# Optimization experiments

Hardware: AMD Instinct MI355X
Metric: run time of the kernel (lower is better)

## Reference

```python
import jax, jax.numpy as jnp
import numpy as np

N_NODES = 50000
N_EDGES = 800000
F_IN = 64
HID = 64
N_CLASSES = 10
N_GRAPHS = 64


def setup_inputs() -> dict:
    key = jax.random.key(0)
    ks = jax.random.split(key, 16)
    x = jax.random.normal(ks[0], (N_NODES, F_IN), dtype=jnp.float32)
    edge_index = jax.random.randint(ks[1], (2, N_EDGES), 0, N_NODES, dtype=jnp.int32)
    supernode_mask = jax.random.bernoulli(ks[2], 0.1, (N_NODES,))
    edge_mask = jax.random.bernoulli(ks[3], 0.5, (N_EDGES,)).astype(jnp.float32)
    batch = jnp.sort(jax.random.randint(ks[4], (N_NODES,), 0, N_GRAPHS, dtype=jnp.int32))
    def glorot(k, fan_in, fan_out):
        s = jnp.sqrt(6.0 / (fan_in + fan_out))
        return jax.random.uniform(k, (fan_in, fan_out), jnp.float32, -s, s)
    W1 = glorot(ks[5], F_IN, HID); b1 = jnp.zeros((HID,), jnp.float32)
    W2 = glorot(ks[6], HID, HID); b2 = jnp.zeros((HID,), jnp.float32)
    W3 = glorot(ks[7], HID, HID); b3 = jnp.zeros((HID,), jnp.float32)
    Wl = glorot(ks[8], HID, N_CLASSES); bl = jnp.zeros((N_CLASSES,), jnp.float32)
    return {"x": x, "edge_index": edge_index, "supernode_mask": supernode_mask,
            "edge_mask": edge_mask, "batch": batch,
            "W1": W1, "b1": b1, "W2": W2, "b2": b2, "W3": W3, "b3": b3,
            "Wl": Wl, "bl": bl}


def reference(x, edge_index, supernode_mask, edge_mask, batch,
              W1, b1, W2, b2, W3, b3, Wl, bl):
    N = x.shape[0]
    src, dst = edge_index[0], edge_index[1]

    # SimpleConv('add'): weighted sum of source features into targets
    x2 = jax.ops.segment_sum(x[src] * edge_mask[:, None], dst, num_segments=N)
    x = jnp.where(supernode_mask[:, None], x2, x)

    # GCN normalization with self-loops: deg = 1 + in-degree, norm = d^-1/2[src]*d^-1/2[dst]
    deg = jax.ops.segment_sum(jnp.ones((src.shape[0],), x.dtype), dst, num_segments=N) + 1.0
    dinv = jax.lax.rsqrt(deg)
    coef = dinv[src] * dinv[dst]          # [E]
    self_coef = (dinv * dinv)[:, None]    # self-loop contribution [N,1]

    def gcn(h, W, b):
        h = h @ W  # small GEMM [N, HID]
        agg = jax.ops.segment_sum(h[src] * coef[:, None], dst, num_segments=N)
        return agg + h * self_coef + b

    h = jax.nn.relu(gcn(x, W1, b1))
    h = jax.nn.relu(gcn(h, W2, b2))
    h = gcn(h, W3, b3)

    # global_mean_pool over graphs
    sums = jax.ops.segment_sum(h, batch, num_segments=N_GRAPHS)
    cnt = jax.ops.segment_sum(jnp.ones((N,), h.dtype), batch, num_segments=N_GRAPHS)
    pooled = sums / jnp.maximum(cnt, 1.0)[:, None]

    # dropout is identity in eval mode
    return pooled @ Wl + bl
```

## Files before the change

kernel.cpp:

```cpp
#include <hip/hip_runtime.h>

#define FEAT 64
#define NGRAPH 64
#define POOL_CHUNKS 8
#define LAYER_BLOCKS 2048


__device__ __forceinline__ unsigned int pack_bf16(float a, float b) {
    unsigned int ua = __float_as_uint(a), ub = __float_as_uint(b);
    ua = (ua + 0x7FFFu + ((ua >> 16) & 1u)) >> 16;
    ub = (ub + 0x7FFFu + ((ub >> 16) & 1u)) >> 16;
    return ua | (ub << 16);
}
__device__ __forceinline__ float bf_lo(unsigned int w) {
    return __uint_as_float(w << 16);
}
__device__ __forceinline__ float bf_hi(unsigned int w) {
    return __uint_as_float(w & 0xFFFF0000u);
}

__global__ __launch_bounds__(256) void k_init(int* __restrict__ cnt_int,
                                              float* __restrict__ pooled,
                                              int* __restrict__ flag, int N) {
    int i = blockIdx.x * 256 + threadIdx.x;
    if (i < N) cnt_int[i] = 0;
    if (i < NGRAPH * FEAT) pooled[i] = 0.f;
    if (i == 0) *flag = 0;
}

__global__ __launch_bounds__(256) void k_detect(const unsigned int* __restrict__ m,
                                                int nwords, int* __restrict__ flag) {
    int i = blockIdx.x * 256 + threadIdx.x;
    if (i >= nwords) return;
    unsigned int w = m[i];
    if (w == 0x3F800000u) atomicOr(flag, 2);
    else if (w > 1u) atomicOr(flag, 1);
}

__device__ __forceinline__ bool read_mask(const void* sm, int i, int fl) {
    if (fl & 2) return ((const float*)sm)[i] != 0.f;
    if (fl & 1) return ((const unsigned char*)sm)[i] != 0;
    return ((const int*)sm)[i] != 0;
}

__global__ __launch_bounds__(256) void k_count(const int* __restrict__ ei,
                                               int* __restrict__ cnt_int,
                                               int* __restrict__ rank, int E) {
    int e = blockIdx.x * 256 + threadIdx.x;
    if (e >= E) return;
    rank[e] = atomicAdd(&cnt_int[ei[E + e]], 1);
}

__global__ __launch_bounds__(256) void k_scan1(const int* __restrict__ cnt,
                                               int* __restrict__ rowptr,
                                               int* __restrict__ bsum, int N) {
    __shared__ int woff[4];
    int t = threadIdx.x, lane = t & 63, wid = t >> 6;
    int i = blockIdx.x * 256 + t;
    int orig = (i < N) ? cnt[i] : 0;
    int v = orig;
#pragma unroll
    for (int off = 1; off < 64; off <<= 1) {
        int u = __shfl_up(v, off);
        if (lane >= off) v += u;
    }
    if (lane == 63) woff[wid] = v;
    __syncthreads();
    if (t == 0) {
        int a = 0;
#pragma unroll
        for (int w = 0; w < 4; ++w) { int b = woff[w]; woff[w] = a; a += b; }
    }
    __syncthreads();
    int excl = woff[wid] + v - orig;
    if (i < N) rowptr[i] = excl;
    if (t == 255) bsum[blockIdx.x] = woff[3] + v;
}

__global__ __launch_bounds__(256) void k_scan2(int* __restrict__ bsum, int nb) {
    __shared__ int woff[4];
    int t = threadIdx.x, lane = t & 63, wid = t >> 6;
    int orig = (t < nb) ? bsum[t] : 0;
    int v = orig;
#pragma unroll
    for (int off = 1; off < 64; off <<= 1) {
        int u = __shfl_up(v, off);
        if (lane >= off) v += u;
    }
    if (lane == 63) woff[wid] = v;
    __syncthreads();
    if (t == 0) {
        int a = 0;
#pragma unroll
        for (int w = 0; w < 4; ++w) { int b = woff[w]; woff[w] = a; a += b; }
    }
    __syncthreads();
    if (t < nb) bsum[t] = woff[wid] + v - orig;
}

__global__ __launch_bounds__(256) void k_scan3(const int* __restrict__ cnt,
                                               const int* __restrict__ bsum,
                                               int* __restrict__ rowptr,
                                               float* __restrict__ dinv,
                                               int N, int E) {
    int i = blockIdx.x * 256 + threadIdx.x;
    if (i >= N) return;
    rowptr[i] += bsum[blockIdx.x];
    dinv[i] = rsqrtf((float)cnt[i] + 1.0f);
    if (i == 0) rowptr[N] = E;
}

__global__ __launch_bounds__(256) void k_fill(const int* __restrict__ ei,
                                              const float* __restrict__ emask,
                                              const int* __restrict__ rowptr,
                                              const int* __restrict__ rank,
                                              unsigned int* __restrict__ csr, int E) {
    int e = blockIdx.x * 256 + threadIdx.x;
    if (e >= E) return;
    int dst = ei[E + e];
    unsigned int word = (unsigned int)ei[e];
    if (emask[e] != 0.f) word |= 0x10000u;
    csr[rowptr[dst] + rank[e]] = word;
}

__global__ __launch_bounds__(256) void k_sup(const float* __restrict__ x,
                                             const int* __restrict__ rowptr,
                                             const unsigned int* __restrict__ csr,
                                             const void* __restrict__ sm,
                                             const int* __restrict__ flag,
                                             const float* __restrict__ dinv,
                                             unsigned int* __restrict__ u, int N) {
    int t = blockIdx.x * 256 + threadIdx.x;
    int i = t >> 6, lane = t & 63;
    if (i >= N) return;
    int g = lane >> 4, q = lane & 15;
    int fl = *flag;
    float4 acc;
    if (read_mask(sm, i, fl)) {
        int r0 = rowptr[i], r1 = rowptr[i + 1];
        acc.x = 0.f; acc.y = 0.f; acc.z = 0.f; acc.w = 0.f;
        for (int j0 = r0; j0 < r1; j0 += 64) {
            int cnt = min(64, r1 - j0);
            unsigned int w_l = (lane < cnt) ? csr[j0 + lane] : 0u;
            int rounds4 = (cnt + 3) & ~3;
#pragma unroll 2
            for (int j = 0; j < rounds4; j += 4) {
                unsigned int wd = __shfl(w_l, j + g);
                if (wd & 0x10000u) {
                    int s = (int)(wd & 0xFFFFu);
                    const float4 v = *(const float4*)(x + (size_t)s * FEAT + q * 4);
                    acc.x += v.x; acc.y += v.y; acc.z += v.z; acc.w += v.w;
                }
            }
        }
#pragma unroll
        for (int m = 16; m < 64; m <<= 1) {
            acc.x += __shfl_xor(acc.x, m);
            acc.y += __shfl_xor(acc.y, m);
            acc.z += __shfl_xor(acc.z, m);
            acc.w += __shfl_xor(acc.w, m);
        }
    } else {
        acc = *(const float4*)(x + (size_t)i * FEAT + q * 4);
    }
    if (g == 0) {
        float dd = dinv[i];
        uint2 p;
        p.x = pack_bf16(acc.x * dd, acc.y * dd);
        p.y = pack_bf16(acc.z * dd, acc.w * dd);
        *(uint2*)(u + (size_t)i * 32 + q * 2) = p;
    }
}

__global__ __launch_bounds__(256, 4) void k_layer(const unsigned int* __restrict__ u,
                                                  const float* __restrict__ W,
                                                  const float* __restrict__ bias,
                                                  const float* __restrict__ dinv,
                                                  const int* __restrict__ rowptr,
                                                  const unsigned int* __restrict__ csr,
                                                  unsigned int* __restrict__ u_out,
                                                  float* __restrict__ h_out,
                                                  int N, int mode) {
    __shared__ float s_lds[4][64];
    int t = threadIdx.x, lane = t & 63, wid = t >> 6;
    int g = lane >> 4, q = lane & 15;
    float w[64];
#pragma unroll
    for (int k = 0; k < 64; ++k) w[k] = W[k * 64 + lane];
    float bl_ = bias[lane];
    for (int i = blockIdx.x * 4 + wid; i < N; i += LAYER_BLOCKS * 4) {
        int r0 = rowptr[i], r1 = rowptr[i + 1];
        float4 acc = {0.f, 0.f, 0.f, 0.f};
        if (g == 0) {
            const uint2 v = *(const uint2*)(u + (size_t)i * 32 + q * 2);
            acc.x += bf_lo(v.x); acc.y += bf_hi(v.x);
            acc.z += bf_lo(v.y); acc.w += bf_hi(v.y);
        }
        for (int j0 = r0; j0 < r1; j0 += 64) {
            int cnt = min(64, r1 - j0);
            int s_l = (lane < cnt) ? (int)(csr[j0 + lane] & 0xFFFFu) : 0;
            int rounds4 = (cnt + 3) & ~3;
#pragma unroll 4
            for (int j = 0; j < rounds4; j += 4) {
                int jj = j + g;
                int s = __shfl(s_l, jj);
                if (jj < cnt) {
                    const uint2 v = *(const uint2*)(u + (size_t)s * 32 + q * 2);
                    acc.x += bf_lo(v.x); acc.y += bf_hi(v.x);
                    acc.z += bf_lo(v.y); acc.w += bf_hi(v.y);
                }
            }
        }
#pragma unroll
        for (int m = 16; m < 64; m <<= 1) {
            acc.x += __shfl_xor(acc.x, m);
            acc.y += __shfl_xor(acc.y, m);
            acc.z += __shfl_xor(acc.z, m);
            acc.w += __shfl_xor(acc.w, m);
        }
        if (g == 0) *(float4*)(&s_lds[wid][q * 4]) = acc;
        float y = 0.f;
#pragma unroll
        for (int k4 = 0; k4 < 16; ++k4) {
            const float4 sv = *(const float4*)(&s_lds[wid][k4 * 4]);
            y += sv.x * w[k4 * 4 + 0] + sv.y * w[k4 * 4 + 1] +
                 sv.z * w[k4 * 4 + 2] + sv.w * w[k4 * 4 + 3];
        }
        float dd = dinv[i];
        y = y * dd + bl_;
        if (mode == 0) {
            y = fmaxf(y, 0.f);
            float up = y * dd;
            float other = __shfl_xor(up, 1);
            if ((lane & 1) == 0)
                u_out[(size_t)i * 32 + (lane >> 1)] = pack_bf16(up, other);
        } else {
            h_out[(size_t)i * FEAT + lane] = y;
        }
    }
}

__device__ __forceinline__ int lbound(const int* a, int n, int key) {
    int lo = 0, hi = n;
    while (lo < hi) {
        int mid = (lo + hi) >> 1;
        if (a[mid] < key) lo = mid + 1; else hi = mid;
    }
    return lo;
}

__global__ __launch_bounds__(256) void k_pool(const float* __restrict__ xbuf,
                                              const int* __restrict__ batch,
                                              float* __restrict__ pooled,
                                              float* __restrict__ gcnt, int N) {
    int g = blockIdx.x >> 3, c = blockIdx.x & (POOL_CHUNKS - 1);
    int lo = lbound(batch, N, g);
    int hi = lbound(batch, N, g + 1);
    int len = hi - lo;
    int t = threadIdx.x, lane = t & 63, sub = t >> 6;
    if (c == 0 && t == 0) gcnt[g] = (float)len;
    int a = lo + (int)(((long long)len * c) / POOL_CHUNKS);
    int bnd = lo + (int)(((long long)len * (c + 1)) / POOL_CHUNKS);
    float s = 0.f;
    for (int i = a + sub; i < bnd; i += 4) s += xbuf[(size_t)i * FEAT + lane];
    __shared__ float red[4][64];
    red[sub][lane] = s;
    __syncthreads();
    if (sub == 0) {
        float tot = red[0][lane] + red[1][lane] + red[2][lane] + red[3][lane];
        unsafeAtomicAdd(&pooled[g * FEAT + lane], tot);
    }
}

__global__ __launch_bounds__(640) void k_logits(const float* __restrict__ pooled,
                                                const float* __restrict__ gcnt,
                                                const float* __restrict__ Wl,
                                                const float* __restrict__ bl,
                                                float* __restrict__ out) {
    int t = threadIdx.x;
    if (t >= NGRAPH * 10) return;
    int g = t / 10, cls = t % 10;
    float inv = 1.f / fmaxf(gcnt[g], 1.f);
    float s = 0.f;
#pragma unroll
    for (int f = 0; f < 64; ++f) s += pooled[g * 64 + f] * Wl[f * 10 + cls];
    out[t] = s * inv + bl[cls];
}

extern "C" void kernel_launch(void* const* d_in, const int* in_sizes, int n_in,
                              void* d_out, int out_size, void* d_ws, size_t ws_size,
                              hipStream_t stream) {
    const float* x = (const float*)d_in[0];
    const int* ei = (const int*)d_in[1];
    const void* sm = d_in[2];
    const float* emask = (const float*)d_in[3];
    const int* batch = (const int*)d_in[4];
    const float* W1 = (const float*)d_in[5];
    const float* b1 = (const float*)d_in[6];
    const float* W2 = (const float*)d_in[7];
    const float* b2 = (const float*)d_in[8];
    const float* W3 = (const float*)d_in[9];
    const float* b3 = (const float*)d_in[10];
    const float* Wl = (const float*)d_in[11];
    const float* bl = (const float*)d_in[12];

    const int N = in_sizes[0] / FEAT;
    const int E = in_sizes[1] / 2;

    float* wsf = (float*)d_ws;
    size_t off = 0;
    float* xbuf = wsf + off;          off += (size_t)N * FEAT;
    unsigned int* u = (unsigned int*)(wsf + off);  off += (size_t)N * 32;
    unsigned int* u2 = (unsigned int*)(wsf + off); off += (size_t)N * 32;
    int* rowptr = (int*)(wsf + off);  off += N + 1;
    int* rank = (int*)(wsf + off);    off += E;
    int* cnt_int = (int*)(wsf + off); off += N;
    float* dinv = wsf + off;          off += N;
    int* bsum = (int*)(wsf + off);    off += 256;
    unsigned int* csr = (unsigned int*)(wsf + off); off += E;
    float* pooled = wsf + off;        off += NGRAPH * FEAT;
    float* gcnt = wsf + off;          off += NGRAPH;
    int* flag = (int*)(wsf + off);

    const int nblocks = (N + 255) / 256;
    const int eblocks = (E + 255) / 256;
    const int wblocks = (N * 64 + 255) / 256;
    const int detect_blocks = (N / 4 + 255) / 256;

    k_init<<<nblocks, 256, 0, stream>>>(cnt_int, pooled, flag, N);
    k_detect<<<detect_blocks, 256, 0, stream>>>((const unsigned int*)sm, N / 4, flag);
    k_count<<<eblocks, 256, 0, stream>>>(ei, cnt_int, rank, E);
    k_scan1<<<nblocks, 256, 0, stream>>>(cnt_int, rowptr, bsum, N);
    k_scan2<<<1, 256, 0, stream>>>(bsum, nblocks);
    k_scan3<<<nblocks, 256, 0, stream>>>(cnt_int, bsum, rowptr, dinv, N, E);
    k_fill<<<eblocks, 256, 0, stream>>>(ei, emask, rowptr, rank, csr, E);
    k_sup<<<wblocks, 256, 0, stream>>>(x, rowptr, csr, sm, flag, dinv, u, N);

    k_layer<<<LAYER_BLOCKS, 256, 0, stream>>>(u, W1, b1, dinv, rowptr, csr,
                                              u2, (float*)nullptr, N, 0);
    k_layer<<<LAYER_BLOCKS, 256, 0, stream>>>(u2, W2, b2, dinv, rowptr, csr,
                                              u, (float*)nullptr, N, 0);
    k_layer<<<LAYER_BLOCKS, 256, 0, stream>>>(u, W3, b3, dinv, rowptr, csr,
                                              (unsigned int*)nullptr, xbuf, N, 1);

    k_pool<<<NGRAPH * POOL_CHUNKS, 256, 0, stream>>>(xbuf, batch, pooled, gcnt, N);
    k_logits<<<1, 640, 0, stream>>>(pooled, gcnt, Wl, bl, (float*)d_out);
}
```

Before: 239.4 us.

## Split GCN layers into MFMA bf16 transform then CSR gather-aggregate

Each fused per-node layer kernel, which aggregated then applied W with scalar FMAs from 64 registers per lane, is replaced by two kernels. The first is a bf16 MFMA GEMM that computes dinv-scaled h@W into a bf16 buffer. The second is a separate gather kernel that sums neighbour rows, adds the self term, and applies bias and ReLU. Weights are pre-transposed and converted to bf16 once. This trades the register-heavy scalar matvec for matrix cores, at the cost of extra launches, an extra N×64 bf16 round trip per layer, and bf16 rounding of the weights.

Measured after the change: 215.5 us. 1.11x faster.

```diff
diff --git a/kernel.cpp b/kernel.cpp
--- a/kernel.cpp
+++ b/kernel.cpp
@@ -3,7 +3,10 @@
 #define FEAT 64
 #define NGRAPH 64
 #define POOL_CHUNKS 8
-#define LAYER_BLOCKS 2048
+
+typedef short bf16x8 __attribute__((ext_vector_type(8)));
+typedef float f32x4 __attribute__((ext_vector_type(4)));
+union FragU { uint4 u4; bf16x8 h; };
 
 
 __device__ __forceinline__ unsigned int pack_bf16(float a, float b) {
@@ -26,6 +29,18 @@
     if (i < N) cnt_int[i] = 0;
     if (i < NGRAPH * FEAT) pooled[i] = 0.f;
     if (i == 0) *flag = 0;
+}
+
+__global__ __launch_bounds__(256) void k_wcvt(const float* __restrict__ W1,
+                                              const float* __restrict__ W2,
+                                              const float* __restrict__ W3,
+                                              unsigned int* __restrict__ wt) {
+    int t = blockIdx.x * 256 + threadIdx.x;
+    if (t >= 3 * 2048) return;
+    int m = t >> 11, w = t & 2047;
+    int c = w >> 5, kw = w & 31;
+    const float* W = (m == 0) ? W1 : ((m == 1) ? W2 : W3);
+    wt[t] = pack_bf16(W[(2 * kw) * 64 + c], W[(2 * kw + 1) * 64 + c]);
 }
 
 __global__ __launch_bounds__(256) void k_detect(const unsigned int* __restrict__ m,
@@ -128,7 +143,6 @@
                                              const unsigned int* __restrict__ csr,
                                              const void* __restrict__ sm,
                                              const int* __restrict__ flag,
-                                             const float* __restrict__ dinv,
                                              unsigned int* __restrict__ u, int N) {
     int t = blockIdx.x * 256 + threadIdx.x;
     int i = t >> 6, lane = t & 63;
@@ -164,78 +178,110 @@
         acc = *(const float4*)(x + (size_t)i * FEAT + q * 4);
     }
     if (g == 0) {
+        uint2 p;
+        p.x = pack_bf16(acc.x, acc.y);
+        p.y = pack_bf16(acc.z, acc.w);
+        *(uint2*)(u + (size_t)i * 32 + q * 2) = p;
+    }
+}
+
+__global__ __launch_bounds__(256) void k_gemm_mfma(const unsigned int* __restrict__ u_in,
+                                                   const unsigned int* __restrict__ wbfT,
+                                                   const float* __restrict__ dinv,
+                                                   unsigned int* __restrict__ hd, int N) {
+    int wid = threadIdx.x >> 6, lane = threadIdx.x & 63;
+    int row0 = (blockIdx.x * 4 + wid) * 16;
+    if (row0 >= N) return;
+    int r = lane & 15, half = lane >> 4;
+    f32x4 acc0 = {0.f, 0.f, 0.f, 0.f}, acc1 = acc0, acc2 = acc0, acc3 = acc0;
+#pragma unroll
+    for (int ks = 0; ks < 2; ++ks) {
+        FragU a;
+        a.u4 = *(const uint4*)(u_in + (size_t)(row0 + r) * 32 + ks * 16 + half * 4);
+        FragU b0, b1, b2, b3;
+        b0.u4 = *(const uint4*)(wbfT + (0 * 16 + r) * 32 + ks * 16 + half * 4);
+        b1.u4 = *(const uint4*)(wbfT + (1 * 16 + r) * 32 + ks * 16 + half * 4);
+        b2.u4 = *(const uint4*)(wbfT + (2 * 16 + r) * 32 + ks * 16 + half * 4);
+        b3.u4 = *(const uint4*)(wbfT + (3 * 16 + r) * 32 + ks * 16 + half * 4);
+        acc0 = __builtin_amdgcn_mfma_f32_16x16x32_bf16(a.h, b0.h, acc0, 0, 0, 0);
+        acc1 = __builtin_amdgcn_mfma_f32_16x16x32_bf16(a.h, b1.h, acc1, 0, 0, 0);
+        acc2 = __builtin_amdgcn_mfma_f32_16x16x32_bf16(a.h, b2.h, acc2, 0, 0, 0);
+        acc3 = __builtin_amdgcn_mfma_f32_16x16x32_bf16(a.h, b3.h, acc3, 0, 0, 0);
+    }
+    float dd0 = dinv[row0 + half * 4 + 0];
+    float dd1 = dinv[row0 + half * 4 + 1];
+    float dd2 = dinv[row0 + half * 4 + 2];
+    float dd3 = dinv[row0 + half * 4 + 3];
+#pragma unroll
+    for (int t = 0; t < 4; ++t) {
+        const f32x4 acc = (t == 0) ? acc0 : (t == 1) ? acc1 : (t == 2) ? acc2 : acc3;
+        float v0 = acc[0] * dd0, v1 = acc[1] * dd1, v2 = acc[2] * dd2, v3 = acc[3] * dd3;
+        float o0 = __shfl_xor(v0, 1), o1 = __shfl_xor(v1, 1),
+              o2 = __shfl_xor(v2, 1), o3 = __shfl_xor(v3, 1);
+        if ((r & 1) == 0) {
+            size_t base = (size_t)(row0 + half * 4) * 32 + t * 8 + (r >> 1);
+            hd[base + 0 * 32] = pack_bf16(v0, o0);
+            hd[base + 1 * 32] = pack_bf16(v1, o1);
+            hd[base + 2 * 32] = pack_bf16(v2, o2);
+            hd[base + 3 * 32] = pack_bf16(v3, o3);
+        }
+    }
+}
+
+__global__ __launch_bounds__(256) void k_gather(const unsigned int* __restrict__ hd,
+                                                const float* __restrict__ b,
+                                                const float* __restrict__ dinv,
+                                                const int* __restrict__ rowptr,
+                                                const unsigned int* __restrict__ csr,
+                                                unsigned int* __restrict__ u_out,
+                                                float* __restrict__ h_out,
+                                                int N, int mode) {
+    int t = blockIdx.x * 256 + threadIdx.x;
+    int i = t >> 6, lane = t & 63;
+    if (i >= N) return;
+    int g = lane >> 4, q = lane & 15;
+    int r0 = rowptr[i], r1 = rowptr[i + 1];
+    float4 acc = {0.f, 0.f, 0.f, 0.f};
+    for (int j0 = r0; j0 < r1; j0 += 64) {
+        int cnt = min(64, r1 - j0);
+        int s_l = (lane < cnt) ? (int)(csr[j0 + lane] & 0xFFFFu) : 0;
+        int rounds4 = (cnt + 3) & ~3;
+#pragma unroll 4
+        for (int j = 0; j < rounds4; j += 4) {
+            int jj = j + g;
+            int s = __shfl(s_l, jj);
+            if (jj < cnt) {
+                const uint2 v = *(const uint2*)(hd + (size_t)s * 32 + q * 2);
+                acc.x += bf_lo(v.x); acc.y += bf_hi(v.x);
+                acc.z += bf_lo(v.y); acc.w += bf_hi(v.y);
+            }
+        }
+    }
+#pragma unroll
+    for (int m = 16; m < 64; m <<= 1) {
+        acc.x += __shfl_xor(acc.x, m);
+        acc.y += __shfl_xor(acc.y, m);
+        acc.z += __shfl_xor(acc.z, m);
+        acc.w += __shfl_xor(acc.w, m);
+    }
+    if (g == 0) {
         float dd = dinv[i];
-        uint2 p;
-        p.x = pack_bf16(acc.x * dd, acc.y * dd);
-        p.y = pack_bf16(acc.z * dd, acc.w * dd);
-        *(uint2*)(u + (size_t)i * 32 + q * 2) = p;
-    }
-}
-
-__global__ __launch_bounds__(256, 4) void k_layer(const unsigned int* __restrict__ u,
-                                                  const float* __restrict__ W,
-                                                  const float* __restrict__ bias,
-                                                  const float* __restrict__ dinv,
-                                                  const int* __restrict__ rowptr,
-                                                  const unsigned int* __restrict__ csr,
-                                                  unsigned int* __restrict__ u_out,
-                                                  float* __restrict__ h_out,
-                                                  int N, int mode) {
-    __shared__ float s_lds[4][64];
-    int t = threadIdx.x, lane = t & 63, wid = t >> 6;
-    int g = lane >> 4, q = lane & 15;
-    float w[64];
-#pragma unroll
-    for (int k = 0; k < 64; ++k) w[k] = W[k * 64 + lane];
-    float bl_ = bias[lane];
-    for (int i = blockIdx.x * 4 + wid; i < N; i += LAYER_BLOCKS * 4) {
-        int r0 = rowptr[i], r1 = rowptr[i + 1];
-        float4 acc = {0.f, 0.f, 0.f, 0.f};
-        if (g == 0) {
-            const uint2 v = *(const uint2*)(u + (size_t)i * 32 + q * 2);
-            acc.x += bf_lo(v.x); acc.y += bf_hi(v.x);
-            acc.z += bf_lo(v.y); acc.w += bf_hi(v.y);
-        }
-        for (int j0 = r0; j0 < r1; j0 += 64) {
-            int cnt = min(64, r1 - j0);
-            int s_l = (lane < cnt) ? (int)(csr[j0 + lane] & 0xFFFFu) : 0;
-            int rounds4 = (cnt + 3) & ~3;
-#pragma unroll 4
-            for (int j = 0; j < rounds4; j += 4) {
-                int jj = j + g;
-                int s = __shfl(s_l, jj);
-                if (jj < cnt) {
-                    const uint2 v = *(const uint2*)(u + (size_t)s * 32 + q * 2);
-                    acc.x += bf_lo(v.x); acc.y += bf_hi(v.x);
-                    acc.z += bf_lo(v.y); acc.w += bf_hi(v.y);
-                }
-            }
-        }
-#pragma unroll
-        for (int m = 16; m < 64; m <<= 1) {
-            acc.x += __shfl_xor(acc.x, m);
-            acc.y += __shfl_xor(acc.y, m);
-            acc.z += __shfl_xor(acc.z, m);
-            acc.w += __shfl_xor(acc.w, m);
-        }
-        if (g == 0) *(float4*)(&s_lds[wid][q * 4]) = acc;
-        float y = 0.f;
-#pragma unroll
-        for (int k4 = 0; k4 < 16; ++k4) {
-            const float4 sv = *(const float4*)(&s_lds[wid][k4 * 4]);
-            y += sv.x * w[k4 * 4 + 0] + sv.y * w[k4 * 4 + 1] +
-                 sv.z * w[k4 * 4 + 2] + sv.w * w[k4 * 4 + 3];
-        }
-        float dd = dinv[i];
-        y = y * dd + bl_;
+        const uint2 hv = *(const uint2*)(hd + (size_t)i * 32 + q * 2);
+        const float4 bv = *(const float4*)(b + q * 4);
+        float4 r;
+        r.x = (acc.x + bf_lo(hv.x)) * dd + bv.x;
+        r.y = (acc.y + bf_hi(hv.x)) * dd + bv.y;
+        r.z = (acc.z + bf_lo(hv.y)) * dd + bv.z;
+        r.w = (acc.w + bf_hi(hv.y)) * dd + bv.w;
         if (mode == 0) {
-            y = fmaxf(y, 0.f);
-            float up = y * dd;
-            float other = __shfl_xor(up, 1);
-            if ((lane & 1) == 0)
-                u_out[(size_t)i * 32 + (lane >> 1)] = pack_bf16(up, other);
+            r.x = fmaxf(r.x, 0.f); r.y = fmaxf(r.y, 0.f);
+            r.z = fmaxf(r.z, 0.f); r.w = fmaxf(r.w, 0.f);
+            uint2 p;
+            p.x = pack_bf16(r.x, r.y);
+            p.y = pack_bf16(r.z, r.w);
+            *(uint2*)(u_out + (size_t)i * 32 + q * 2) = p;
         } else {
-            h_out[(size_t)i * FEAT + lane] = y;
+            *(float4*)(h_out + (size_t)i * FEAT + q * 4) = r;
         }
     }
 }
@@ -310,8 +356,10 @@
     float* wsf = (float*)d_ws;
     size_t off = 0;
     float* xbuf = wsf + off;          off += (size_t)N * FEAT;
-    unsigned int* u = (unsigned int*)(wsf + off);  off += (size_t)N * 32;
-    unsigned int* u2 = (unsigned int*)(wsf + off); off += (size_t)N * 32;
+    unsigned int* ua = (unsigned int*)(wsf + off); off += (size_t)N * 32;
+    unsigned int* ub = (unsigned int*)(wsf + off); off += (size_t)N * 32;
+    unsigned int* hd = (unsigned int*)(wsf + off); off += (size_t)N * 32;
+    unsigned int* wbf = (unsigned int*)(wsf + off); off += 3 * 2048;
     int* rowptr = (int*)(wsf + off);  off += N + 1;
     int* rank = (int*)(wsf + off);    off += E;
     int* cnt_int = (int*)(wsf + off); off += N;
@@ -325,23 +373,25 @@
     const int nblocks = (N + 255) / 256;
     const int eblocks = (E + 255) / 256;
     const int wblocks = (N * 64 + 255) / 256;
+    const int gemm_blocks = (N / 16 + 3) / 4;
     const int detect_blocks = (N / 4 + 255) / 256;
 
     k_init<<<nblocks, 256, 0, stream>>>(cnt_int, pooled, flag, N);
+    k_wcvt<<<24, 256, 0, stream>>>(W1, W2, W3, wbf);
     k_detect<<<detect_blocks, 256, 0, stream>>>((const unsigned int*)sm, N / 4, flag);
     k_count<<<eblocks, 256, 0, stream>>>(ei, cnt_int, rank, E);
     k_scan1<<<nblocks, 256, 0, stream>>>(cnt_int, rowptr, bsum, N);
     k_scan2<<<1, 256, 0, stream>>>(bsum, nblocks);
     k_scan3<<<nblocks, 256, 0, stream>>>(cnt_int, bsum, rowptr, dinv, N, E);
     k_fill<<<eblocks, 256, 0, stream>>>(ei, emask, rowptr, rank, csr, E);
-    k_sup<<<wblocks, 256, 0, stream>>>(x, rowptr, csr, sm, flag, dinv, u, N);
-
-    k_layer<<<LAYER_BLOCKS, 256, 0, stream>>>(u, W1, b1, dinv, rowptr, csr,
-                                              u2, (float*)nullptr, N, 0);
-    k_layer<<<LAYER_BLOCKS, 256, 0, stream>>>(u2, W2, b2, dinv, rowptr, csr,
-                                              u, (float*)nullptr, N, 0);
-    k_layer<<<LAYER_BLOCKS, 256, 0, stream>>>(u, W3, b3, dinv, rowptr, csr,
-                                              (unsigned int*)nullptr, xbuf, N, 1);
+    k_sup<<<wblocks, 256, 0, stream>>>(x, rowptr, csr, sm, flag, ua, N);
+
+    k_gemm_mfma<<<gemm_blocks, 256, 0, stream>>>(ua, wbf + 0 * 2048, dinv, hd, N);
+    k_gather<<<wblocks, 256, 0, stream>>>(hd, b1, dinv, rowptr, csr, ub, (float*)nullptr, N, 0);
+    k_gemm_mfma<<<gemm_blocks, 256, 0, stream>>>(ub, wbf + 1 * 2048, dinv, hd, N);
+    k_gather<<<wblocks, 256, 0, stream>>>(hd, b2, dinv, rowptr, csr, ua, (float*)nullptr, N, 0);
+    k_gemm_mfma<<<gemm_blocks, 256, 0, stream>>>(ua, wbf + 2 * 2048, dinv, hd, N);
+    k_gather<<<wblocks, 256, 0, stream>>>(hd, b3, dinv, rowptr, csr, (unsigned int*)nullptr, xbuf, N, 1);
 
     k_pool<<<NGRAPH * POOL_CHUNKS, 256, 0, stream>>>(xbuf, batch, pooled, gcnt, N);
     k_logits<<<1, 640, 0, stream>>>(pooled, gcnt, Wl, bl, (float*)d_out);
```
